# Optimization experiments

Measured on AMD Instinct MI355X. Metric: run time of the kernel, lower is better.

Reference implementation:

```python
import jax, jax.numpy as jnp
import numpy as np

G, NA, C, NMAX = 32, 1024, 4, 6   # graphs, atoms/graph, latent charge channels, k-grid extent
SIGMA = 1.0                        # Gaussian smearing width (Angstrom)
BOX_L = 20.0


def _kgrid_integers(nmax):
    """All integer triples in [-nmax, nmax]^3 excluding the origin. [K, 3]"""
    r = np.arange(-nmax, nmax + 1)
    n = np.stack(np.meshgrid(r, r, r, indexing='ij'), axis=-1).reshape(-1, 3)
    n = n[np.any(n != 0, axis=1)]
    return jnp.asarray(n, dtype=jnp.float32)  # [K=2196, 3]


def setup_inputs() -> dict:
    key = jax.random.key(0)
    k1, k2, k3 = jax.random.split(key, 3)
    pos = jax.random.uniform(k1, (G * NA, 3), dtype=jnp.float32) * BOX_L
    q = jax.random.normal(k2, (G * NA, C), dtype=jnp.float32) * 0.1
    # near-cubic cells with a small random strain (keeps them invertible)
    cell = jnp.eye(3, dtype=jnp.float32) * BOX_L + 0.1 * jax.random.normal(k3, (G, 3, 3), dtype=jnp.float32)
    batch = jnp.repeat(jnp.arange(G, dtype=jnp.int32), NA)  # sorted segment ids
    return {"q": q, "pos": pos, "cell": cell, "batch": batch}


def reference(q, pos, cell, batch):
    """Latent Ewald reciprocal-space sum.

    E_lr[g] = 1/(2 V_g) * sum_{k != 0} 4*pi/k^2 * exp(-sigma^2 k^2 / 2) * sum_c |S_c(k)|^2
    with S_c(k) = sum_{i in graph g} q_ic exp(i k . r_i).

    Segments are equal-sized and sorted (batch = repeat(arange(G), NA)), so the
    per-graph segment reduction is expressed as a reshape + batched einsum.
    """
    del batch  # layout is encoded by the reshape below (equal-sized sorted segments)
    nvec = _kgrid_integers(NMAX)                         # [K, 3]
    # reciprocal lattice rows: b_i with a_i . b_j = 2*pi*delta_ij
    recip = 2.0 * jnp.pi * jnp.swapaxes(jnp.linalg.inv(cell), -1, -2)  # [G, 3, 3]
    kvec = jnp.einsum('kj,gjd->gkd', nvec, recip)        # [G, K, 3]
    k2 = jnp.sum(kvec * kvec, axis=-1)                   # [G, K]
    vol = jnp.abs(jnp.linalg.det(cell))                  # [G]

    posg = pos.reshape(G, NA, 3)
    qg = q.reshape(G, NA, C)

    phase = jnp.einsum('gnd,gkd->gnk', posg, kvec)       # [G, NA, K]
    cosph = jnp.cos(phase)
    sinph = jnp.sin(phase)
    s_re = jnp.einsum('gnc,gnk->gkc', qg, cosph)         # [G, K, C]
    s_im = jnp.einsum('gnc,gnk->gkc', qg, sinph)
    s2 = jnp.sum(s_re * s_re + s_im * s_im, axis=-1)     # [G, K]

    w = 4.0 * jnp.pi * jnp.exp(-0.5 * (SIGMA ** 2) * k2) / jnp.maximum(k2, 1e-12)
    e_lr = jnp.sum(w * s2, axis=-1) / (2.0 * vol)        # [G]
    return e_lr
```

## Files before the change

### kernel.cpp

```cpp
#include <hip/hip_runtime.h>
#include <math.h>

#define G      32
#define NA     1024
#define C      4
#define NMAX   6
#define KHALF  1098
#define KSLICES 18
#define WAVES  8
#define BLOCK  (WAVES * 64)
#define ATOMS_PER_WAVE (NA / WAVES)

__global__ __launch_bounds__(BLOCK)
void ewald_recip_kernel(const float* __restrict__ q,
                        const float* __restrict__ pos,
                        const float* __restrict__ cell,
                        float* __restrict__ out)
{
    __shared__ __align__(16) float s_atom[NA][8];
    __shared__ float s_red[WAVES][64][8];

    const int b    = blockIdx.x;
    const int g    = b / KSLICES;
    const int ks   = b % KSLICES;
    const int t    = threadIdx.x;
    const int wave = t >> 6;
    const int lane = t & 63;

    const float* posg = pos + (size_t)g * NA * 3;
    const float* qg   = q   + (size_t)g * NA * 4;
    for (int a = t; a < NA; a += BLOCK) {
        float px = posg[a * 3 + 0];
        float py = posg[a * 3 + 1];
        float pz = posg[a * 3 + 2];
        const float4 qa = *reinterpret_cast<const float4*>(qg + (size_t)a * 4);
        s_atom[a][0] = px; s_atom[a][1] = py; s_atom[a][2] = pz; s_atom[a][3] = 0.f;
        s_atom[a][4] = qa.x; s_atom[a][5] = qa.y; s_atom[a][6] = qa.z; s_atom[a][7] = qa.w;
    }

    const float* M = cell + (size_t)g * 9;
    const float m00 = M[0], m01 = M[1], m02 = M[2];
    const float m10 = M[3], m11 = M[4], m12 = M[5];
    const float m20 = M[6], m21 = M[7], m22 = M[8];
    const float c00 =  (m11 * m22 - m12 * m21);
    const float c01 = -(m10 * m22 - m12 * m20);
    const float c02 =  (m10 * m21 - m11 * m20);
    const float c10 = -(m01 * m22 - m02 * m21);
    const float c11 =  (m00 * m22 - m02 * m20);
    const float c12 = -(m00 * m21 - m01 * m20);
    const float c20 =  (m01 * m12 - m02 * m11);
    const float c21 = -(m00 * m12 - m02 * m10);
    const float c22 =  (m00 * m11 - m01 * m10);
    const float det    = m00 * c00 + m01 * c01 + m02 * c02;
    const float invdet = 1.0f / det;

    const int  kk    = ks * 64 + lane;
    const bool valid = (kk < KHALF);
    int n1, n2, n3;
    if (kk < 1014) {
        n1 = 1 + kk / 169;
        const int r = kk - (n1 - 1) * 169;
        n2 = r / 13 - 6;
        n3 = r - (r / 13) * 13 - 6;
    } else if (kk < 1092) {
        const int j = kk - 1014;
        n1 = 0;
        n2 = 1 + j / 13;
        n3 = j - (j / 13) * 13 - 6;
    } else {
        n1 = 0; n2 = 0;
        n3 = kk - 1091;
    }
    const float fn1 = (float)n1, fn2 = (float)n2, fn3 = (float)n3;

    const float kr0 = (fn1 * c00 + fn2 * c10 + fn3 * c20) * invdet;
    const float kr1 = (fn1 * c01 + fn2 * c11 + fn3 * c21) * invdet;
    const float kr2 = (fn1 * c02 + fn2 * c12 + fn3 * c22) * invdet;

    __syncthreads();

    float sr0 = 0.f, sr1 = 0.f, sr2 = 0.f, sr3 = 0.f;
    float si0 = 0.f, si1 = 0.f, si2 = 0.f, si3 = 0.f;
    const int a0 = wave * ATOMS_PER_WAVE;
    #pragma unroll 4
    for (int a = 0; a < ATOMS_PER_WAVE; ++a) {
        const float* at = s_atom[a0 + a];
        const float4 pp = *reinterpret_cast<const float4*>(at);
        const float4 qa = *reinterpret_cast<const float4*>(at + 4);
        const float ph = pp.x * kr0 + pp.y * kr1 + pp.z * kr2;
        const float u  = __builtin_amdgcn_fractf(ph);
        const float sn = __builtin_amdgcn_sinf(u);
        const float cs = __builtin_amdgcn_cosf(u);
        sr0 = fmaf(qa.x, cs, sr0);  si0 = fmaf(qa.x, sn, si0);
        sr1 = fmaf(qa.y, cs, sr1);  si1 = fmaf(qa.y, sn, si1);
        sr2 = fmaf(qa.z, cs, sr2);  si2 = fmaf(qa.z, sn, si2);
        sr3 = fmaf(qa.w, cs, sr3);  si3 = fmaf(qa.w, sn, si3);
    }

    {
        float* rp = s_red[wave][lane];
        rp[0] = sr0; rp[1] = sr1; rp[2] = sr2; rp[3] = sr3;
        rp[4] = si0; rp[5] = si1; rp[6] = si2; rp[7] = si3;
    }
    __syncthreads();

    if (t < 64) {
        float r0 = 0.f, r1 = 0.f, r2 = 0.f, r3 = 0.f;
        float i0 = 0.f, i1 = 0.f, i2 = 0.f, i3 = 0.f;
        #pragma unroll
        for (int w = 0; w < WAVES; ++w) {
            const float* p = s_red[w][lane];
            r0 += p[0]; r1 += p[1]; r2 += p[2]; r3 += p[3];
            i0 += p[4]; i1 += p[5]; i2 += p[6]; i3 += p[7];
        }
        const float s2 = r0 * r0 + r1 * r1 + r2 * r2 + r3 * r3
                       + i0 * i0 + i1 * i1 + i2 * i2 + i3 * i3;
        const float kk2 = kr0 * kr0 + kr1 * kr1 + kr2 * kr2;
        const float fourpi2 = 4.0f * (float)M_PI * (float)M_PI;
        const float k2 = fourpi2 * kk2;
        const float wt = 4.0f * (float)M_PI * __expf(-0.5f * k2) / fmaxf(k2, 1e-12f);
        float contrib = valid ? wt * s2 : 0.0f;
        #pragma unroll
        for (int off = 32; off > 0; off >>= 1)
            contrib += __shfl_down(contrib, off, 64);
        if (lane == 0)
            atomicAdd(&out[g], contrib * fabsf(invdet));
    }
}

extern "C" void kernel_launch(void* const* d_in, const int* in_sizes, int n_in,
                              void* d_out, int out_size, void* d_ws, size_t ws_size,
                              hipStream_t stream) {
    const float* q    = (const float*)d_in[0];
    const float* pos  = (const float*)d_in[1];
    const float* cell = (const float*)d_in[2];
    float* out = (float*)d_out;

    hipMemsetAsync(out, 0, G * sizeof(float), stream);

    dim3 grid(G * KSLICES);
    dim3 block(BLOCK);
    ewald_recip_kernel<<<grid, block, 0, stream>>>(q, pos, cell, out);
}
```

Baseline: 82.40 us.

## Prepack atoms into global workspace and drop LDS staging; use packed FMAs

```diff
diff --git a/kernel.cpp b/kernel.cpp
--- a/kernel.cpp
+++ b/kernel.cpp
@@ -9,15 +9,31 @@
 #define KSLICES 18
 #define WAVES  8
 #define BLOCK  (WAVES * 64)
-#define ATOMS_PER_WAVE (NA / WAVES)
+#define APW    (NA / WAVES)
+
+typedef float f32x2 __attribute__((ext_vector_type(2)));
+typedef float f32x4 __attribute__((ext_vector_type(4)));
+
+__global__ __launch_bounds__(256)
+void prepack_kernel(const float* __restrict__ q,
+                    const float* __restrict__ pos,
+                    float* __restrict__ ws)
+{
+    const int a = blockIdx.x * 256 + threadIdx.x;
+    if (a < G * NA) {
+        f32x4 p4 = { pos[a * 3 + 0], pos[a * 3 + 1], pos[a * 3 + 2], 0.f };
+        const f32x4 qa = *reinterpret_cast<const f32x4*>(q + (size_t)a * 4);
+        f32x4* w = reinterpret_cast<f32x4*>(ws + (size_t)a * 8);
+        w[0] = p4;
+        w[1] = qa;
+    }
+}
 
 __global__ __launch_bounds__(BLOCK)
-void ewald_recip_kernel(const float* __restrict__ q,
-                        const float* __restrict__ pos,
+void ewald_recip_kernel(const float* __restrict__ ws,
                         const float* __restrict__ cell,
                         float* __restrict__ out)
 {
-    __shared__ __align__(16) float s_atom[NA][8];
     __shared__ float s_red[WAVES][64][8];
 
     const int b    = blockIdx.x;
@@ -26,17 +42,6 @@
     const int t    = threadIdx.x;
     const int wave = t >> 6;
     const int lane = t & 63;
-
-    const float* posg = pos + (size_t)g * NA * 3;
-    const float* qg   = q   + (size_t)g * NA * 4;
-    for (int a = t; a < NA; a += BLOCK) {
-        float px = posg[a * 3 + 0];
-        float py = posg[a * 3 + 1];
-        float pz = posg[a * 3 + 2];
-        const float4 qa = *reinterpret_cast<const float4*>(qg + (size_t)a * 4);
-        s_atom[a][0] = px; s_atom[a][1] = py; s_atom[a][2] = pz; s_atom[a][3] = 0.f;
-        s_atom[a][4] = qa.x; s_atom[a][5] = qa.y; s_atom[a][6] = qa.z; s_atom[a][7] = qa.w;
-    }
 
     const float* M = cell + (size_t)g * 9;
     const float m00 = M[0], m01 = M[1], m02 = M[2];
@@ -77,30 +82,35 @@
     const float kr1 = (fn1 * c01 + fn2 * c11 + fn3 * c21) * invdet;
     const float kr2 = (fn1 * c02 + fn2 * c12 + fn3 * c22) * invdet;
 
-    __syncthreads();
-
-    float sr0 = 0.f, sr1 = 0.f, sr2 = 0.f, sr3 = 0.f;
-    float si0 = 0.f, si1 = 0.f, si2 = 0.f, si3 = 0.f;
-    const int a0 = wave * ATOMS_PER_WAVE;
-    #pragma unroll 4
-    for (int a = 0; a < ATOMS_PER_WAVE; ++a) {
-        const float* at = s_atom[a0 + a];
-        const float4 pp = *reinterpret_cast<const float4*>(at);
-        const float4 qa = *reinterpret_cast<const float4*>(at + 4);
-        const float ph = pp.x * kr0 + pp.y * kr1 + pp.z * kr2;
-        const float u  = __builtin_amdgcn_fractf(ph);
-        const float sn = __builtin_amdgcn_sinf(u);
-        const float cs = __builtin_amdgcn_cosf(u);
-        sr0 = fmaf(qa.x, cs, sr0);  si0 = fmaf(qa.x, sn, si0);
-        sr1 = fmaf(qa.y, cs, sr1);  si1 = fmaf(qa.y, sn, si1);
-        sr2 = fmaf(qa.z, cs, sr2);  si2 = fmaf(qa.z, sn, si2);
-        sr3 = fmaf(qa.w, cs, sr3);  si3 = fmaf(qa.w, sn, si3);
+    f32x2 aR01 = {0.f, 0.f}, aR23 = {0.f, 0.f};
+    f32x2 aI01 = {0.f, 0.f}, aI23 = {0.f, 0.f};
+    {
+        const int a0 = wave * APW;
+        const f32x4* rec = reinterpret_cast<const f32x4*>(ws) +
+                           (size_t)2 * ((size_t)g * NA + a0);
+        #pragma unroll 4
+        for (int a = 0; a < APW; ++a) {
+            const f32x4 pp = rec[2 * a];
+            const f32x4 qa = rec[2 * a + 1];
+            const float ph = fmaf(pp.x, kr0, fmaf(pp.y, kr1, pp.z * kr2));
+            const float u  = __builtin_amdgcn_fractf(ph);
+            const float sn = __builtin_amdgcn_sinf(u);
+            const float cs = __builtin_amdgcn_cosf(u);
+            const f32x2 cs2 = {cs, cs};
+            const f32x2 sn2 = {sn, sn};
+            const f32x2 q01 = {qa.x, qa.y};
+            const f32x2 q23 = {qa.z, qa.w};
+            aR01 = __builtin_elementwise_fma(q01, cs2, aR01);
+            aR23 = __builtin_elementwise_fma(q23, cs2, aR23);
+            aI01 = __builtin_elementwise_fma(q01, sn2, aI01);
+            aI23 = __builtin_elementwise_fma(q23, sn2, aI23);
+        }
     }
 
     {
         float* rp = s_red[wave][lane];
-        rp[0] = sr0; rp[1] = sr1; rp[2] = sr2; rp[3] = sr3;
-        rp[4] = si0; rp[5] = si1; rp[6] = si2; rp[7] = si3;
+        rp[0] = aR01.x; rp[1] = aR01.y; rp[2] = aR23.x; rp[3] = aR23.y;
+        rp[4] = aI01.x; rp[5] = aI01.y; rp[6] = aI23.x; rp[7] = aI23.y;
     }
     __syncthreads();
 
@@ -135,10 +145,13 @@
     const float* pos  = (const float*)d_in[1];
     const float* cell = (const float*)d_in[2];
     float* out = (float*)d_out;
+    float* ws  = (float*)d_ws;
 
     hipMemsetAsync(out, 0, G * sizeof(float), stream);
 
+    prepack_kernel<<<(G * NA + 255) / 256, 256, 0, stream>>>(q, pos, ws);
+
     dim3 grid(G * KSLICES);
     dim3 block(BLOCK);
-    ewald_recip_kernel<<<grid, block, 0, stream>>>(q, pos, cell, out);
+    ewald_recip_kernel<<<grid, block, 0, stream>>>(ws, cell, out);
 }
```

After: 107.4 us. 1.3x slower.
